# Kernel tuning notes

Hardware: AMD Instinct MI355X
Metric: run time of the kernel (lower is better)

## Reference

```python
import jax, jax.numpy as jnp
import numpy as np

B, L, DIM = 2, 2048, 2048
N_HEADS, N_KV_HEADS = 32, 8
HEAD_DIM = DIM // N_HEADS  # 64
SCALE = HEAD_DIM ** -0.5


def setup_inputs() -> dict:
    key = jax.random.key(0)
    ks = jax.random.split(key, 6)
    s = 0.02
    x = jax.random.normal(ks[0], (B, L, DIM), dtype=jnp.float32)
    wq = jax.random.normal(ks[1], (N_HEADS * HEAD_DIM, DIM), dtype=jnp.float32) * s
    wk = jax.random.normal(ks[2], (N_KV_HEADS * HEAD_DIM, DIM), dtype=jnp.float32) * s
    wv = jax.random.normal(ks[3], (N_KV_HEADS * HEAD_DIM, DIM), dtype=jnp.float32) * s
    wo = jax.random.normal(ks[4], (DIM, N_HEADS * HEAD_DIM), dtype=jnp.float32) * s
    # standard RoPE frequencies: theta = 10000^(-2i/d), angle = pos * theta
    inv_freq = 1.0 / (10000.0 ** (jnp.arange(0, HEAD_DIM, 2, dtype=jnp.float32) / HEAD_DIM))
    angles = jnp.arange(L, dtype=jnp.float32)[:, None] * inv_freq[None, :]  # [L, HEAD_DIM//2]
    freqs_cos = jnp.cos(angles)
    freqs_sin = jnp.sin(angles)
    # additive causal mask [1, 1, L, L]
    causal = jnp.tril(jnp.ones((L, L), dtype=bool))
    mask = jnp.where(causal, 0.0, -1e9).astype(jnp.float32)[None, None]
    return {"x": x, "wq": wq, "wk": wk, "wv": wv, "wo": wo,
            "freqs_cos": freqs_cos, "freqs_sin": freqs_sin, "mask": mask}


def _apply_rope(t, cos, sin):
    # t: [B, H, L, D]; complex pairing is (even, odd) interleaved along D
    te, to = t[..., 0::2], t[..., 1::2]
    cos = cos[None, None, : t.shape[2], :]
    sin = sin[None, None, : t.shape[2], :]
    re = te * cos - to * sin
    im = te * sin + to * cos
    return jnp.stack([re, im], axis=-1).reshape(t.shape)


def reference(x, wq, wk, wv, wo, freqs_cos, freqs_sin, mask):
    b, l, _ = x.shape
    q = (x @ wq.T).reshape(b, l, N_HEADS, HEAD_DIM).transpose(0, 2, 1, 3)
    k = (x @ wk.T).reshape(b, l, N_KV_HEADS, HEAD_DIM).transpose(0, 2, 1, 3)
    v = (x @ wv.T).reshape(b, l, N_KV_HEADS, HEAD_DIM).transpose(0, 2, 1, 3)
    q = _apply_rope(q, freqs_cos, freqs_sin)
    k = _apply_rope(k, freqs_cos, freqs_sin)
    repeats = N_HEADS // N_KV_HEADS
    k = jnp.repeat(k, repeats, axis=1)
    v = jnp.repeat(v, repeats, axis=1)
    scores = jnp.einsum("bhqd,bhkd->bhqk", q, k) * SCALE + mask
    probs = jax.nn.softmax(scores, axis=-1)
    out = jnp.einsum("bhqk,bhkd->bhqd", probs, v)
    out = out.transpose(0, 2, 1, 3).reshape(b, l, N_HEADS * HEAD_DIM)
    return out @ wo.T
```

## Files before the change

### kernel.cpp

```cpp
#include <hip/hip_runtime.h>
#include <hip/hip_bf16.h>
#include <stdint.h>

typedef __attribute__((ext_vector_type(8))) short bf16x8;
typedef __attribute__((ext_vector_type(4))) float f32x4;
typedef __attribute__((ext_vector_type(16))) float f32x16;
typedef __attribute__((ext_vector_type(4))) unsigned int u32x4;

#define B_    2
#define L_    2048
#define DIM_  2048
#define NH_   32
#define NKV_  8
#define HD_   64
#define KVD_  512
#define CLOG_ 0.1803368801111244f

__device__ __forceinline__ unsigned short f2bf(float f) {
  unsigned u = __float_as_uint(f);
  u += 0x7fff + ((u >> 16) & 1);
  return (unsigned short)(u >> 16);
}
__device__ __forceinline__ unsigned cvtpk(float lo, float hi_) {
  unsigned r;
  asm("v_cvt_pk_bf16_f32 %0, %1, %2" : "=v"(r) : "v"(lo), "v"(hi_));
  return r;
}
__device__ __forceinline__ float bf2f(unsigned short h) {
  return __uint_as_float(((unsigned)h) << 16);
}
__device__ __forceinline__ void plswap2(unsigned &a, unsigned &b, int hi) {
#if __has_builtin(__builtin_amdgcn_permlane32_swap)
  auto r = __builtin_amdgcn_permlane32_swap(a, b, false, false);
  a = (unsigned)r[0]; b = (unsigned)r[1];
#else
  unsigned xa = (unsigned)__shfl_xor((int)a, 32);
  unsigned xb = (unsigned)__shfl_xor((int)b, 32);
  unsigned na = hi ? xb : a, nb = hi ? b : xa;
  a = na; b = nb;
#endif
}

#define GLDS16(gsrc, ldst) __builtin_amdgcn_global_load_lds( \
    (const __attribute__((address_space(1))) unsigned int*)(gsrc), \
    (__attribute__((address_space(3))) unsigned int*)(ldst), 16, 0, 0)

__global__ void cvt_all(const float* __restrict__ x,  const float* __restrict__ wq,
                        const float* __restrict__ wk, const float* __restrict__ wv,
                        const float* __restrict__ wo,
                        unsigned short* __restrict__ xb,  unsigned short* __restrict__ wqb,
                        unsigned short* __restrict__ wkb, unsigned short* __restrict__ wvb,
                        unsigned short* __restrict__ wob) {
  int i = blockIdx.x * blockDim.x + threadIdx.x;
  const float* src; unsigned short* dst; int off;
  if (i < 2097152)      { src = x;  dst = xb;  off = i; }
  else if (i < 3145728) { src = wq; dst = wqb; off = i - 2097152; }
  else if (i < 3407872) { src = wk; dst = wkb; off = i - 3145728; }
  else if (i < 3670016) { src = wv; dst = wvb; off = i - 3407872; }
  else                  { src = wo; dst = wob; off = i - 3670016; }
  float4 v = reinterpret_cast<const float4*>(src)[off];
  ushort4 o;
  o.x = f2bf(v.x); o.y = f2bf(v.y); o.z = f2bf(v.z); o.w = f2bf(v.w);
  reinterpret_cast<ushort4*>(dst)[off] = o;
}

template<int OUTMODE>
__device__ __forceinline__ void gemm128_core(
    const unsigned short* __restrict__ A,
    const unsigned short* __restrict__ W,
    void* __restrict__ C, int N, int K, int m0, int n0,
    unsigned short (*As)[128 * 64], unsigned short (*Bs)[128 * 64])
{
  const int tid = threadIdx.x;
  const int lane = tid & 63, wid = tid >> 6;
  const int wm = wid >> 1, wn = wid & 1;
  const int r = lane & 15, g = lane >> 4;
  const int rsw = (r & 7) << 4;
  f32x4 acc[4][4] = {};

  auto STAGE = [&](int buf, int k0) {
#pragma unroll
    for (int p = 0; p < 4; ++p) {
      int off = (p * 256 + tid) * 16;
      int row = off >> 7;
      int colb = (off & 127) ^ ((row & 7) << 4);
      GLDS16((const char*)A + ((size_t)(m0 + row) * K + k0) * 2 + colb,
             (char*)As[buf] + off);
      GLDS16((const char*)W + ((size_t)(n0 + row) * K + k0) * 2 + colb,
             (char*)Bs[buf] + off);
    }
  };

  const int nt = K >> 6;
  STAGE(0, 0);
  asm volatile("s_waitcnt vmcnt(0)" ::: "memory");
  __builtin_amdgcn_s_barrier();
  int cur = 0;
  for (int kt = 0; kt < nt; ++kt) {
    if (kt + 1 < nt) {
      STAGE(cur ^ 1, (kt + 1) << 6);
      asm volatile("s_waitcnt vmcnt(8)" ::: "memory");
    } else {
      asm volatile("s_waitcnt vmcnt(0)" ::: "memory");
    }
    __builtin_amdgcn_s_barrier();
    __builtin_amdgcn_sched_barrier(0);
    const char* Ab = (const char*)As[cur];
    const char* Bb = (const char*)Bs[cur];
    __builtin_amdgcn_s_setprio(1);
#pragma unroll
    for (int kk = 0; kk < 2; ++kk) {
      bf16x8 af[4], bfv[4];
#pragma unroll
      for (int i = 0; i < 4; ++i)
        af[i] = *reinterpret_cast<const bf16x8*>(
            Ab + (wm * 64 + i * 16 + r) * 128 + ((kk * 64 + g * 16) ^ rsw));
#pragma unroll
      for (int i = 0; i < 4; ++i)
        bfv[i] = *reinterpret_cast<const bf16x8*>(
            Bb + (wn * 64 + i * 16 + r) * 128 + ((kk * 64 + g * 16) ^ rsw));
#pragma unroll
      for (int i = 0; i < 4; ++i)
#pragma unroll
        for (int j = 0; j < 4; ++j)
          acc[i][j] = __builtin_amdgcn_mfma_f32_16x16x32_bf16(af[i], bfv[j], acc[i][j], 0, 0, 0);
    }
    __builtin_amdgcn_s_setprio(0);
    asm volatile("s_waitcnt lgkmcnt(0)" ::: "memory");
    __builtin_amdgcn_s_barrier();
    cur ^= 1;
  }

  if (OUTMODE == 2) {
#pragma unroll
    for (int i = 0; i < 4; ++i)
#pragma unroll
      for (int jf = 0; jf < 4; ++jf) {
        int col = n0 + wn * 64 + jf * 16 + r;
        int kvi = col >> 6, d = col & 63;
        int tok = m0 + wm * 64 + i * 16 + g * 4;
        int bb = tok >> 11, tl = tok & (L_ - 1);
        uint2 u;
        u.x = cvtpk(acc[i][jf][0], acc[i][jf][1]);
        u.y = cvtpk(acc[i][jf][2], acc[i][jf][3]);
        *reinterpret_cast<uint2*>((unsigned short*)C +
            ((size_t)((bb * NKV_ + kvi) * HD_ + d)) * L_ + tl) = u;
      }
  } else {
#pragma unroll
    for (int i = 0; i < 4; ++i)
#pragma unroll
      for (int jf = 0; jf < 4; ++jf)
#pragma unroll
        for (int j = 0; j < 4; ++j) {
          size_t row = (size_t)(m0 + wm * 64 + i * 16 + g * 4 + j);
          size_t col = (size_t)(n0 + wn * 64 + jf * 16 + r);
          float v = acc[i][jf][j];
          if (OUTMODE == 1) ((float*)C)[row * N + col] = v;
          else ((unsigned short*)C)[row * N + col] = f2bf(v);
        }
  }
}

template<int OUT_F32>
__global__ __launch_bounds__(256) void gemm_bt(
    const unsigned short* __restrict__ A,
    const unsigned short* __restrict__ W,
    void* __restrict__ C, int M, int N, int K)
{
  __shared__ unsigned short As[2][128 * 64];
  __shared__ unsigned short Bs[2][128 * 64];
  gemm128_core<OUT_F32 ? 1 : 0>(A, W, C, N, K, blockIdx.y * 128, blockIdx.x * 128, As, Bs);
}

__global__ __launch_bounds__(256) void gemm_qkv(
    const unsigned short* __restrict__ A,
    const unsigned short* __restrict__ Wq,
    const unsigned short* __restrict__ Wk,
    const unsigned short* __restrict__ Wv,
    unsigned short* __restrict__ Cq,
    unsigned short* __restrict__ Ck,
    unsigned short* __restrict__ Vt)
{
  __shared__ unsigned short As[2][128 * 64];
  __shared__ unsigned short Bs[2][128 * 64];
  const int bx = blockIdx.x;
  const int m0 = blockIdx.y * 128;
  if (bx < 16)
    gemm128_core<0>(A, Wq, Cq, 2048, DIM_, m0, bx * 128, As, Bs);
  else if (bx < 20)
    gemm128_core<0>(A, Wk, Ck, 512, DIM_, m0, (bx - 16) * 128, As, Bs);
  else
    gemm128_core<2>(A, Wv, Vt, 512, DIM_, m0, (bx - 20) * 128, As, Bs);
}

__global__ void rope_v8(unsigned short* __restrict__ t,
                        const float* __restrict__ fc,
                        const float* __restrict__ fs,
                        int rowElems, int lshift, float scale) {
  int idx = blockIdx.x * blockDim.x + threadIdx.x;
  int row = idx >> lshift;
  if (row >= B_ * L_) return;
  int pos = (idx & ((1 << lshift) - 1)) << 3;
  int l = row & (L_ - 1);
  int i0 = (pos & 63) >> 1;
  unsigned short* p = t + (size_t)row * rowElems + pos;
  uint4 v = *reinterpret_cast<const uint4*>(p);
  float4 c4 = *reinterpret_cast<const float4*>(fc + l * 32 + i0);
  float4 s4 = *reinterpret_cast<const float4*>(fs + l * 32 + i0);
  float cc[4] = {c4.x * scale, c4.y * scale, c4.z * scale, c4.w * scale};
  float ss[4] = {s4.x * scale, s4.y * scale, s4.z * scale, s4.w * scale};
  unsigned wds[4] = {v.x, v.y, v.z, v.w};
  uint4 o;
  unsigned ow[4];
#pragma unroll
  for (int k = 0; k < 4; ++k) {
    float te = bf2f((unsigned short)(wds[k] & 0xffff));
    float to = bf2f((unsigned short)(wds[k] >> 16));
    ow[k] = cvtpk(te * cc[k] - to * ss[k], te * ss[k] + to * cc[k]);
  }
  o.x = ow[0]; o.y = ow[1]; o.z = ow[2]; o.w = ow[3];
  *reinterpret_cast<uint4*>(p) = o;
}

__global__ __launch_bounds__(128) void attn_kernel(
    const unsigned short* __restrict__ Q,
    const unsigned short* __restrict__ K,
    const unsigned short* __restrict__ Vt,
    unsigned short* __restrict__ AO)
{
  __shared__ unsigned short Ks[2][64 * 64];
  __shared__ unsigned short Vs[2][64 * 64];
  const int tid = threadIdx.x;
  const int lane = tid & 63, w = tid >> 6;
  const int ql = lane & 31;
  const int hi = lane >> 5;
  const int wid = blockIdx.x;
  const int c = wid >> 6;
  const int bh = wid & 63;
  const int bse = (c >> 3) * 4 + (c & 3);
  const int qt = (c & 4) ? (31 - bse) : bse;
  const int b = bh >> 5, h = bh & 31, kv = h >> 2;
  const int qw = qt * 64 + w * 32;
  const int nkt = qt + 1;

  bf16x8 qf[4];
  const unsigned short* qbase = Q + ((size_t)(b * L_ + qw + ql)) * DIM_ + h * HD_ + hi * 8;
#pragma unroll
  for (int dk = 0; dk < 4; ++dk)
    qf[dk] = *reinterpret_cast<const bf16x8*>(qbase + dk * 16);

  const unsigned short* Kg = K + (size_t)b * L_ * KVD_ + kv * HD_;
  const unsigned short* Vg = Vt + ((size_t)(b * NKV_ + kv)) * HD_ * L_;

  f32x16 oacc0 = {}, oacc1 = {};
  float lrow = 0.f;
  const int rsw = (ql & 7) << 4;

  auto STAGE = [&](int buf, int t) {
    const int k0 = t * 64;
#pragma unroll
    for (int p = 0; p < 4; ++p) {
      int off = (p * 128 + tid) * 16;
      int row = off >> 7;
      int colb = (off & 127) ^ ((row & 7) << 4);
      GLDS16((const char*)Kg + ((size_t)(k0 + row)) * (KVD_ * 2) + colb,
             (char*)Ks[buf] + off);
      GLDS16((const char*)Vg + ((size_t)row) * (L_ * 2) + (size_t)k0 * 2 + colb,
             (char*)Vs[buf] + off);
    }
  };

  int cur = 0;
  STAGE(0, 0);
  asm volatile("s_waitcnt vmcnt(0)" ::: "memory");
  __builtin_amdgcn_s_barrier();

  for (int t = 0; t < nkt; ++t) {
    if (t + 1 < nkt) {
      STAGE(cur ^ 1, t + 1);
      asm volatile("s_waitcnt vmcnt(8)" ::: "memory");
    } else {
      asm volatile("s_waitcnt vmcnt(0)" ::: "memory");
    }
    __builtin_amdgcn_s_barrier();
    __builtin_amdgcn_sched_barrier(0);
    const int k0 = t * 64;
    {
      const char* Kl = (const char*)Ks[cur];
      const char* Vl = (const char*)Vs[cur];
      f32x16 s0 = {}, s1 = {};
      __builtin_amdgcn_s_setprio(1);
#pragma unroll
      for (int dk = 0; dk < 4; ++dk) {
        bf16x8 kf0 = *reinterpret_cast<const bf16x8*>(Kl + ql * 128 + ((dk * 32 + hi * 16) ^ rsw));
        bf16x8 kf1 = *reinterpret_cast<const bf16x8*>(Kl + (32 + ql) * 128 + ((dk * 32 + hi * 16) ^ rsw));
        s0 = __builtin_amdgcn_mfma_f32_32x32x16_bf16(kf0, qf[dk], s0, 0, 0, 0);
        s1 = __builtin_amdgcn_mfma_f32_32x32x16_bf16(kf1, qf[dk], s1, 0, 0, 0);
      }
      __builtin_amdgcn_s_setprio(0);
      float p[32];
      float ps = 0.f;
      if (k0 + 63 > qw) {
        int q = qw + ql;
#pragma unroll
        for (int i = 0; i < 32; ++i) {
          float sv = (i < 16) ? s0[i] : s1[i - 16];
          int kk = k0 + (i >> 4) * 32 + (i & 3) + 8 * ((i & 15) >> 2) + 4 * hi;
          float e = exp2f(sv);
          e = (kk > q) ? 0.f : e;
          p[i] = e; ps += e;
        }
      } else {
#pragma unroll
        for (int i = 0; i < 32; ++i) {
          float sv = (i < 16) ? s0[i] : s1[i - 16];
          p[i] = exp2f(sv); ps += p[i];
        }
      }
      lrow += ps;
      bf16x8 pf[4];
#pragma unroll
      for (int s = 0; s < 4; ++s) {
        int bp = ((s >> 1) << 4) + ((s & 1) << 3);
        unsigned w0 = cvtpk(p[bp + 0], p[bp + 1]);
        unsigned w1 = cvtpk(p[bp + 2], p[bp + 3]);
        unsigned w2 = cvtpk(p[bp + 4], p[bp + 5]);
        unsigned w3 = cvtpk(p[bp + 6], p[bp + 7]);
        plswap2(w0, w2, hi);
        plswap2(w1, w3, hi);
        u32x4 fw;
        fw[0] = w0; fw[1] = w1; fw[2] = w2; fw[3] = w3;
        pf[s] = __builtin_bit_cast(bf16x8, fw);
      }
      __builtin_amdgcn_s_setprio(1);
#pragma unroll
      for (int s = 0; s < 4; ++s) {
        bf16x8 v0 = *reinterpret_cast<const bf16x8*>(Vl + ql * 128 + ((s * 32 + hi * 16) ^ rsw));
        bf16x8 v1 = *reinterpret_cast<const bf16x8*>(Vl + (32 + ql) * 128 + ((s * 32 + hi * 16) ^ rsw));
        oacc0 = __builtin_amdgcn_mfma_f32_32x32x16_bf16(v0, pf[s], oacc0, 0, 0, 0);
        oacc1 = __builtin_amdgcn_mfma_f32_32x32x16_bf16(v1, pf[s], oacc1, 0, 0, 0);
      }
      __builtin_amdgcn_s_setprio(0);
    }
    asm volatile("s_waitcnt lgkmcnt(0)" ::: "memory");
    __builtin_amdgcn_s_barrier();
    cur ^= 1;
  }

  unsigned la = __float_as_uint(lrow), lb = __float_as_uint(lrow);
  plswap2(la, lb, hi);
  float ltot = __uint_as_float(la) + __uint_as_float(lb);
  float inv = 1.f / ltot;
  unsigned short* obase = AO + ((size_t)(b * L_ + qw + ql)) * DIM_ + h * HD_;
#pragma unroll
  for (int g4 = 0; g4 < 4; ++g4) {
    uint2 u;
    u.x = cvtpk(oacc0[g4 * 4 + 0] * inv, oacc0[g4 * 4 + 1] * inv);
    u.y = cvtpk(oacc0[g4 * 4 + 2] * inv, oacc0[g4 * 4 + 3] * inv);
    *reinterpret_cast<uint2*>(obase + g4 * 8 + hi * 4) = u;
    uint2 v;
    v.x = cvtpk(oacc1[g4 * 4 + 0] * inv, oacc1[g4 * 4 + 1] * inv);
    v.y = cvtpk(oacc1[g4 * 4 + 2] * inv, oacc1[g4 * 4 + 3] * inv);
    *reinterpret_cast<uint2*>(obase + 32 + g4 * 8 + hi * 4) = v;
  }
}

extern "C" void kernel_launch(void* const* d_in, const int* in_sizes, int n_in,
                              void* d_out, int out_size, void* d_ws, size_t ws_size,
                              hipStream_t stream) {
  const float* x  = (const float*)d_in[0];
  const float* wq = (const float*)d_in[1];
  const float* wk = (const float*)d_in[2];
  const float* wv = (const float*)d_in[3];
  const float* wo = (const float*)d_in[4];
  const float* fc = (const float*)d_in[5];
  const float* fs = (const float*)d_in[6];
  float* out = (float*)d_out;

  unsigned short* ws  = (unsigned short*)d_ws;
  unsigned short* xb  = ws;
  unsigned short* wqb = xb  + 8388608;
  unsigned short* wkb = wqb + 4194304;
  unsigned short* wvb = wkb + 1048576;
  unsigned short* wob = wvb + 1048576;
  unsigned short* Qb  = wob + 4194304;
  unsigned short* Kb  = Qb  + 8388608;
  unsigned short* Vtb = Kb  + 2097152;
  unsigned short* AOb = Vtb + 2097152;

  cvt_all<<<18432, 256, 0, stream>>>(x, wq, wk, wv, wo, xb, wqb, wkb, wvb, wob);

  gemm_qkv<<<dim3(24, 32), 256, 0, stream>>>(xb, wqb, wkb, wvb, Qb, Kb, Vtb);

  rope_v8<<<4096, 256, 0, stream>>>(Qb, fc, fs, 2048, 8, CLOG_);
  rope_v8<<<1024, 256, 0, stream>>>(Kb, fc, fs, 512, 6, 1.0f);

  attn_kernel<<<2048, 128, 0, stream>>>(Qb, Kb, Vtb, AOb);

  gemm_bt<1><<<dim3(16, 32), 256, 0, stream>>>(AOb, wob, out, 4096, 2048, 2048);
}
```

Baseline: 232.9 us.

## Fuse Q RoPE into attention and enlarge blocks to 256 query rows

Removes the separate RoPE pass over Q by applying rotary embedding and the softmax scale while loading Q fragments inside the attention kernel. Attention blocks grow from 2 to 8 waves, each covering 256 query rows that share the staged K/V tiles, and block indices pair light and heavy causal chunks to balance work. Waves skip tiles lying entirely above their causal diagonal. Larger blocks cut redundant K/V global loads but make waves within a block wait at barriers for tiles they skip, and lower the number of blocks available to fill the GPU.

```diff
diff --git a/kernel.cpp b/kernel.cpp
--- a/kernel.cpp
+++ b/kernel.cpp
@@ -223,32 +223,51 @@
   *reinterpret_cast<uint4*>(p) = o;
 }
 
-__global__ __launch_bounds__(128) void attn_kernel(
+__global__ __launch_bounds__(512, 4) void attn_kernel(
     const unsigned short* __restrict__ Q,
     const unsigned short* __restrict__ K,
     const unsigned short* __restrict__ Vt,
+    const float* __restrict__ fc, const float* __restrict__ fs,
     unsigned short* __restrict__ AO)
 {
   __shared__ unsigned short Ks[2][64 * 64];
   __shared__ unsigned short Vs[2][64 * 64];
   const int tid = threadIdx.x;
   const int lane = tid & 63, w = tid >> 6;
-  const int ql = lane & 31;
-  const int hi = lane >> 5;
-  const int wid = blockIdx.x;
-  const int c = wid >> 6;
-  const int bh = wid & 63;
-  const int bse = (c >> 3) * 4 + (c & 3);
-  const int qt = (c & 4) ? (31 - bse) : bse;
+  const int ql = lane & 31, hi = lane >> 5;
+  const int id = blockIdx.x;
+  const int pairIdx = id >> 1;
+  const int bh = pairIdx & 63;
+  const int g = pairIdx >> 6;
+  const int c = (id & 1) ? (7 - g) : g;
   const int b = bh >> 5, h = bh & 31, kv = h >> 2;
-  const int qw = qt * 64 + w * 32;
-  const int nkt = qt + 1;
+  const int qw = c * 256 + w * 32;
+  const int nkt = (c + 1) * 4;
 
   bf16x8 qf[4];
-  const unsigned short* qbase = Q + ((size_t)(b * L_ + qw + ql)) * DIM_ + h * HD_ + hi * 8;
-#pragma unroll
-  for (int dk = 0; dk < 4; ++dk)
-    qf[dk] = *reinterpret_cast<const bf16x8*>(qbase + dk * 16);
+  {
+    const unsigned short* qrow = Q + ((size_t)(b * L_ + qw + ql)) * DIM_ + h * HD_;
+    const float* fcr = fc + (size_t)(qw + ql) * 32;
+    const float* fsr = fs + (size_t)(qw + ql) * 32;
+#pragma unroll
+    for (int dk = 0; dk < 4; ++dk) {
+      uint4 v = *reinterpret_cast<const uint4*>(qrow + dk * 16 + hi * 8);
+      float4 c4 = *reinterpret_cast<const float4*>(fcr + dk * 8 + hi * 4);
+      float4 s4 = *reinterpret_cast<const float4*>(fsr + dk * 8 + hi * 4);
+      float cc[4] = {c4.x, c4.y, c4.z, c4.w};
+      float ss[4] = {s4.x, s4.y, s4.z, s4.w};
+      unsigned wd[4] = {v.x, v.y, v.z, v.w};
+      u32x4 o;
+#pragma unroll
+      for (int k2 = 0; k2 < 4; ++k2) {
+        float te = bf2f((unsigned short)(wd[k2] & 0xffff));
+        float to = bf2f((unsigned short)(wd[k2] >> 16));
+        o[k2] = cvtpk((te * cc[k2] - to * ss[k2]) * CLOG_,
+                      (te * ss[k2] + to * cc[k2]) * CLOG_);
+      }
+      qf[dk] = __builtin_bit_cast(bf16x8, o);
+    }
+  }
 
   const unsigned short* Kg = K + (size_t)b * L_ * KVD_ + kv * HD_;
   const unsigned short* Vg = Vt + ((size_t)(b * NKV_ + kv)) * HD_ * L_;
@@ -259,16 +278,13 @@
 
   auto STAGE = [&](int buf, int t) {
     const int k0 = t * 64;
-#pragma unroll
-    for (int p = 0; p < 4; ++p) {
-      int off = (p * 128 + tid) * 16;
-      int row = off >> 7;
-      int colb = (off & 127) ^ ((row & 7) << 4);
-      GLDS16((const char*)Kg + ((size_t)(k0 + row)) * (KVD_ * 2) + colb,
-             (char*)Ks[buf] + off);
-      GLDS16((const char*)Vg + ((size_t)row) * (L_ * 2) + (size_t)k0 * 2 + colb,
-             (char*)Vs[buf] + off);
-    }
+    int off = tid * 16;
+    int row = off >> 7;
+    int colb = (off & 127) ^ ((row & 7) << 4);
+    GLDS16((const char*)Kg + ((size_t)(k0 + row)) * (KVD_ * 2) + colb,
+           (char*)Ks[buf] + off);
+    GLDS16((const char*)Vg + ((size_t)row) * (L_ * 2) + (size_t)k0 * 2 + colb,
+           (char*)Vs[buf] + off);
   };
 
   int cur = 0;
@@ -279,14 +295,14 @@
   for (int t = 0; t < nkt; ++t) {
     if (t + 1 < nkt) {
       STAGE(cur ^ 1, t + 1);
-      asm volatile("s_waitcnt vmcnt(8)" ::: "memory");
+      asm volatile("s_waitcnt vmcnt(2)" ::: "memory");
     } else {
       asm volatile("s_waitcnt vmcnt(0)" ::: "memory");
     }
     __builtin_amdgcn_s_barrier();
     __builtin_amdgcn_sched_barrier(0);
     const int k0 = t * 64;
-    {
+    if (k0 < qw + 32) {
       const char* Kl = (const char*)Ks[cur];
       const char* Vl = (const char*)Vs[cur];
       f32x16 s0 = {}, s1 = {};
@@ -393,10 +409,9 @@
 
   gemm_qkv<<<dim3(24, 32), 256, 0, stream>>>(xb, wqb, wkb, wvb, Qb, Kb, Vtb);
 
-  rope_v8<<<4096, 256, 0, stream>>>(Qb, fc, fs, 2048, 8, CLOG_);
   rope_v8<<<1024, 256, 0, stream>>>(Kb, fc, fs, 512, 6, 1.0f);
 
-  attn_kernel<<<2048, 128, 0, stream>>>(Qb, Kb, Vtb, AOb);
+  attn_kernel<<<512, 512, 0, stream>>>(Qb, Kb, Vtb, fc, fs, AOb);
 
   gemm_bt<1><<<dim3(16, 32), 256, 0, stream>>>(AOb, wob, out, 4096, 2048, 2048);
 }
```

Result: no change. 231.3 us (-0.7%).
